# Performance work log

Measured on AMD Instinct MI355X. Metric: run time of the kernel, lower is better.

Reference implementation:

```python
import jax, jax.numpy as jnp
import numpy as np

B, S, D, H, DFF = 2, 2048, 1024, 16, 4096
DH = D // H
EPS = 1e-8


def _alibi_bias(num_heads, seq_len, dtype=jnp.float32):
    # ALiBi slopes for power-of-two head counts: 2^(-8*(h+1)/H)
    h = jnp.arange(1, num_heads + 1, dtype=dtype)
    slopes = jnp.exp2(-8.0 * h / num_heads)          # [H]
    pos = jnp.arange(seq_len, dtype=dtype)
    rel = jnp.abs(pos[None, :] - pos[:, None])       # [S, S] |i-j|
    return -slopes[:, None, None] * rel[None]        # [H, S, S]


def _rmsnorm(x, scale):
    rms = jax.lax.rsqrt(jnp.mean(x * x, axis=-1, keepdims=True) + EPS)
    return scale * x * rms


def setup_inputs() -> dict:
    key = jax.random.key(0)
    ks = jax.random.split(key, 12)
    sd = 0.02
    return {
        "x": jax.random.normal(ks[0], (B, S, D), jnp.float32),
        "scale1": jnp.ones((D,), jnp.float32),
        "scale2": jnp.ones((D,), jnp.float32),
        "w_qkv": jax.random.normal(ks[1], (D, 3 * D), jnp.float32) * sd,
        "b_qkv": jnp.zeros((3 * D,), jnp.float32),
        "w_out": jax.random.normal(ks[2], (D, D), jnp.float32) * sd,
        "b_out": jnp.zeros((D,), jnp.float32),
        "w1": jax.random.normal(ks[3], (D, DFF), jnp.float32) * sd,
        "b1": jnp.zeros((DFF,), jnp.float32),
        "w2": jax.random.normal(ks[4], (DFF, D), jnp.float32) * sd,
        "b2": jnp.zeros((D,), jnp.float32),
    }


def reference(x, scale1, scale2, w_qkv, b_qkv, w_out, b_out, w1, b1, w2, b2):
    residual = x
    xn = _rmsnorm(x, scale1)
    qkv = xn @ w_qkv + b_qkv                                  # [B,S,3D]
    q, k, v = jnp.split(qkv, 3, axis=-1)
    def heads(t):
        return t.reshape(B, S, H, DH).transpose(0, 2, 1, 3)   # [B,H,S,DH]
    q, k, v = heads(q), heads(k), heads(v)
    scores = jnp.einsum("bhsd,bhtd->bhst", q, k) / (DH ** 0.5)
    scores = scores + _alibi_bias(H, S, scores.dtype)[None]
    attn = jax.nn.softmax(scores, axis=-1)
    out = jnp.einsum("bhst,bhtd->bhsd", attn, v)              # [B,H,S,DH]
    out = out.transpose(0, 2, 1, 3).reshape(B, S, D)
    x = residual + (out @ w_out + b_out)
    residual = x
    xn = _rmsnorm(x, scale2)
    h = jax.nn.gelu(xn @ w1 + b1, approximate=False)
    return residual + (h @ w2 + b2)
```

## Files before the change

kernel.cpp:

```cpp
#include <hip/hip_runtime.h>
#include <hip/hip_bf16.h>
#include <math.h>

#define B_ 2
#define S_ 2048
#define D_ 1024
#define H_ 16
#define DH_ 64
#define DFF_ 4096
#define M_ (B_*S_)

typedef __bf16 bf16;
typedef __bf16 bf16x8 __attribute__((ext_vector_type(8)));
typedef __bf16 bf16x4 __attribute__((ext_vector_type(4)));
typedef float f32x4 __attribute__((ext_vector_type(4)));

__device__ __forceinline__ void gll16(const void* g, void* l) {
  __builtin_amdgcn_global_load_lds(
      (const __attribute__((address_space(1))) void*)g,
      (__attribute__((address_space(3))) void*)l, 16, 0, 0);
}

__global__ __launch_bounds__(256) void rmsnorm_kernel(const float* __restrict__ x,
    const float* __restrict__ scale, bf16* __restrict__ out) {
  __shared__ float red[4];
  int row = blockIdx.x, t = threadIdx.x;
  const float4* xr = (const float4*)(x + (size_t)row * D_);
  float4 v = xr[t];
  float ss = v.x*v.x + v.y*v.y + v.z*v.z + v.w*v.w;
  #pragma unroll
  for (int off = 32; off > 0; off >>= 1) ss += __shfl_down(ss, off, 64);
  if ((t & 63) == 0) red[t >> 6] = ss;
  __syncthreads();
  float tot = red[0] + red[1] + red[2] + red[3];
  float r = rsqrtf(tot * (1.0f / D_) + 1e-8f);
  float4 sc = ((const float4*)scale)[t];
  bf16x4 o;
  o[0] = (bf16)(v.x * sc.x * r);
  o[1] = (bf16)(v.y * sc.y * r);
  o[2] = (bf16)(v.z * sc.z * r);
  o[3] = (bf16)(v.w * sc.w * r);
  *(bf16x4*)(out + (size_t)row * D_ + t * 4) = o;
}

__global__ __launch_bounds__(256) void reduce_rms_kernel(
    const bf16* __restrict__ p0, const bf16* __restrict__ p1,
    const float* __restrict__ x, const float* __restrict__ bias,
    const float* __restrict__ scale, float* __restrict__ x2, bf16* __restrict__ xn2) {
  __shared__ float red[4];
  int row = blockIdx.x, t = threadIdx.x;
  float4 xv = ((const float4*)(x + (size_t)row * D_))[t];
  float4 bv = ((const float4*)bias)[t];
  bf16x4 a = *(const bf16x4*)(p0 + (size_t)row * D_ + t * 4);
  bf16x4 b = *(const bf16x4*)(p1 + (size_t)row * D_ + t * 4);
  float s0 = xv.x + bv.x + (float)a[0] + (float)b[0];
  float s1 = xv.y + bv.y + (float)a[1] + (float)b[1];
  float s2 = xv.z + bv.z + (float)a[2] + (float)b[2];
  float s3 = xv.w + bv.w + (float)a[3] + (float)b[3];
  float4 o; o.x = s0; o.y = s1; o.z = s2; o.w = s3;
  ((float4*)(x2 + (size_t)row * D_))[t] = o;
  float ss = s0*s0 + s1*s1 + s2*s2 + s3*s3;
  #pragma unroll
  for (int off = 32; off > 0; off >>= 1) ss += __shfl_down(ss, off, 64);
  if ((t & 63) == 0) red[t >> 6] = ss;
  __syncthreads();
  float tot = red[0] + red[1] + red[2] + red[3];
  float r = rsqrtf(tot * (1.0f / D_) + 1e-8f);
  float4 sc = ((const float4*)scale)[t];
  bf16x4 on;
  on[0] = (bf16)(s0 * sc.x * r);
  on[1] = (bf16)(s1 * sc.y * r);
  on[2] = (bf16)(s2 * sc.z * r);
  on[3] = (bf16)(s3 * sc.w * r);
  *(bf16x4*)(xn2 + (size_t)row * D_ + t * 4) = on;
}

__global__ __launch_bounds__(256) void reduce_out_kernel(
    const bf16* __restrict__ p0, const bf16* __restrict__ p1,
    const float* __restrict__ x2, const float* __restrict__ bias,
    float* __restrict__ dout) {
  int row = blockIdx.x, t = threadIdx.x;
  float4 xv = ((const float4*)(x2 + (size_t)row * D_))[t];
  float4 bv = ((const float4*)bias)[t];
  bf16x4 a = *(const bf16x4*)(p0 + (size_t)row * D_ + t * 4);
  bf16x4 b = *(const bf16x4*)(p1 + (size_t)row * D_ + t * 4);
  float4 o;
  o.x = xv.x + bv.x + (float)a[0] + (float)b[0];
  o.y = xv.y + bv.y + (float)a[1] + (float)b[1];
  o.z = xv.z + bv.z + (float)a[2] + (float)b[2];
  o.w = xv.w + bv.w + (float)a[3] + (float)b[3];
  ((float4*)(dout + (size_t)row * D_))[t] = o;
}

__global__ __launch_bounds__(256) void wtrans_kernel(const float* __restrict__ W,
    bf16* __restrict__ Wt, int K, int N) {
  __shared__ float tile[32][33];
  int n0 = blockIdx.x * 32, k0 = blockIdx.y * 32;
  int tx = threadIdx.x & 31, ty = threadIdx.x >> 5;
  #pragma unroll
  for (int i = 0; i < 4; i++)
    tile[ty + i*8][tx] = W[(size_t)(k0 + ty + i*8) * N + n0 + tx];
  __syncthreads();
  #pragma unroll
  for (int i = 0; i < 4; i++)
    Wt[(size_t)(n0 + ty + i*8) * K + k0 + tx] = (bf16)tile[tx][ty + i*8];
}

__global__ __launch_bounds__(256) void vtrans_kernel(const bf16* __restrict__ Vin,
    bf16* __restrict__ Vt) {
  __shared__ bf16 tile[32][34];
  size_t base = (size_t)blockIdx.z * (S_ * DH_);
  int s0 = blockIdx.x * 32, d0 = blockIdx.y * 32;
  int tx = threadIdx.x & 31, ty = threadIdx.x >> 5;
  #pragma unroll
  for (int i = 0; i < 4; i++)
    tile[ty + i*8][tx] = Vin[base + (size_t)(s0 + ty + i*8) * DH_ + d0 + tx];
  __syncthreads();
  #pragma unroll
  for (int i = 0; i < 4; i++)
    Vt[base + (size_t)(d0 + ty + i*8) * S_ + s0 + tx] = tile[tx][ty + i*8];
}

__device__ __forceinline__ float gelu_exact(float v) {
  return 0.5f * v * (1.0f + erff(v * 0.70710678118654752f));
}

template<int MODE>
__global__ __launch_bounds__(256) void gemm_kernel(
    const bf16* __restrict__ A, const bf16* __restrict__ Bt,
    const float* __restrict__ bias, void* __restrict__ outp, void* __restrict__ outp2,
    int M, int N, int K, int lda) {
  __shared__ __align__(16) bf16 As[128 * 32];
  __shared__ __align__(16) bf16 Bs[128 * 32];
  int t = threadIdx.x;
  int wave = t >> 6, lane = t & 63;
  int lm = lane & 15, lg = lane >> 4;
  int m0 = blockIdx.y * 128, n0 = blockIdx.x * 128;
  size_t koff = (size_t)blockIdx.z * K;
  int wm = (wave >> 1) * 64, wn = (wave & 1) * 64;
  f32x4 acc[4][4] = {};

  const bf16* Ag = A + (size_t)(m0 + (t >> 2)) * lda + koff + (t & 3) * 8;
  const bf16* Bg = Bt + (size_t)(n0 + (t >> 2)) * lda + koff + (t & 3) * 8;

  for (int k0 = 0; k0 < K; k0 += 32) {
    __syncthreads();
    gll16(Ag + k0, As + t * 8);
    gll16(Ag + k0 + (size_t)64 * lda, As + 2048 + t * 8);
    gll16(Bg + k0, Bs + t * 8);
    gll16(Bg + k0 + (size_t)64 * lda, Bs + 2048 + t * 8);
    __syncthreads();
    bf16x8 af[4], bfr[4];
    #pragma unroll
    for (int i = 0; i < 4; i++)
      af[i] = *(const bf16x8*)(As + (wm + i * 16 + lm) * 32 + lg * 8);
    #pragma unroll
    for (int j = 0; j < 4; j++)
      bfr[j] = *(const bf16x8*)(Bs + (wn + j * 16 + lm) * 32 + lg * 8);
    #pragma unroll
    for (int i = 0; i < 4; i++)
      #pragma unroll
      for (int j = 0; j < 4; j++)
        acc[i][j] = __builtin_amdgcn_mfma_f32_16x16x32_bf16(af[i], bfr[j], acc[i][j], 0, 0, 0);
  }

  bf16* pout = (MODE == 5) ? ((blockIdx.z == 0) ? (bf16*)outp : (bf16*)outp2) : (bf16*)outp;

  #pragma unroll
  for (int i = 0; i < 4; i++) {
    int row = m0 + wm + i * 16 + lg * 4;
    #pragma unroll
    for (int j = 0; j < 4; j++) {
      int col = n0 + wn + j * 16 + lm;
      float bcol = (MODE == 5) ? 0.f : bias[col];
      #pragma unroll
      for (int r = 0; r < 4; r++) {
        float v = acc[i][j][r] + bcol;
        int rr = row + r;
        if (MODE == 0) {
          int which = col >> 10, d = col & 1023;
          int hh = d >> 6, dh = d & 63;
          int bb = rr >> 11, s = rr & 2047;
          ((bf16*)outp)[(size_t)which * ((size_t)B_*H_*S_*DH_) +
              ((size_t)(bb * H_ + hh) * S_ + s) * DH_ + dh] = (bf16)v;
        } else if (MODE == 2) {
          ((bf16*)outp)[(size_t)rr * N + col] = (bf16)gelu_exact(v);
        } else {
          pout[(size_t)rr * N + col] = (bf16)v;
        }
      }
    }
  }
}

#define PSTR 68
__global__ __launch_bounds__(256, 3) void attn_kernel(
    const bf16* __restrict__ q, const bf16* __restrict__ k,
    const bf16* __restrict__ vT, bf16* __restrict__ ao) {
  __shared__ __align__(16) bf16 Ks[2][64 * 64];
  __shared__ __align__(16) bf16 Vs[2][64 * 64];
  __shared__ __align__(16) bf16 Ps[4 * 16 * PSTR];
  int t = threadIdx.x, wave = t >> 6, lane = t & 63;
  int lm = lane & 15, lg = lane >> 4;
  int q0 = blockIdx.x * 64;
  int h = blockIdx.y, b = blockIdx.z;
  size_t base = (size_t)(b * H_ + h) * ((size_t)S_ * DH_);
  const bf16* Q = q + base;
  const bf16* K = k + base;
  const bf16* V = vT + base;
  const float LOG2E = 1.4426950408889634f;
  float sl2 = exp2f(-0.5f * (float)(h + 1)) * LOG2E;
  float nslope = -sl2;
  const float qscale = 0.125f * LOG2E;
  const float FMAX = 8.0f;

  int W = (int)(24.0f / sl2);
  int jlo = (q0 - W) >> 6; if (jlo < 0) jlo = 0;
  int jhi = ((q0 + 63 + W) >> 6) + 1; if (jhi > S_ / 64) jhi = S_ / 64;

  bf16x8 qf[2];
  #pragma unroll
  for (int h2 = 0; h2 < 2; h2++) {
    bf16x8 v = *(const bf16x8*)(Q + (size_t)(q0 + wave * 16 + lm) * DH_ + h2 * 32 + lg * 8);
    #pragma unroll
    for (int e = 0; e < 8; e++) v[e] = (bf16)((float)v[e] * qscale);
    qf[h2] = v;
  }

  int row0 = t >> 3, jslot = t & 7;
  int gsw = (jslot ^ (row0 & 7)) << 3;
  const bf16* Ksrc0 = K + (size_t)row0 * DH_ + gsw;
  const bf16* Vsrc0 = V + (size_t)row0 * S_ + gsw;

  {
    int jt = jlo << 6;
    gll16(Ksrc0 + (size_t)jt * DH_, Ks[0] + (size_t)t * 8);
    gll16(Ksrc0 + (size_t)(jt + 32) * DH_, Ks[0] + (size_t)(t + 256) * 8);
    gll16(Vsrc0 + jt, Vs[0] + (size_t)t * 8);
    gll16(Vsrc0 + (size_t)32 * S_ + jt, Vs[0] + (size_t)(t + 256) * 8);
  }

  f32x4 oacc[4] = {};
  float rs[4] = {0.f, 0.f, 0.f, 0.f};
  int psw = lm & 7;

  for (int jj = jlo; jj < jhi; ++jj) {
    int buf = (jj - jlo) & 1;
    int jt = jj << 6;
    __syncthreads();
    if (jj + 1 < jhi) {
      int jn = (jj + 1) << 6;
      gll16(Ksrc0 + (size_t)jn * DH_, Ks[buf ^ 1] + (size_t)t * 8);
      gll16(Ksrc0 + (size_t)(jn + 32) * DH_, Ks[buf ^ 1] + (size_t)(t + 256) * 8);
      gll16(Vsrc0 + jn, Vs[buf ^ 1] + (size_t)t * 8);
      gll16(Vsrc0 + (size_t)32 * S_ + jn, Vs[buf ^ 1] + (size_t)(t + 256) * 8);
    }
    const bf16* Kb = Ks[buf];
    const bf16* Vb = Vs[buf];

    f32x4 sc[4];
    #pragma unroll
    for (int tt = 0; tt < 4; tt++) {
      f32x4 a = {-FMAX, -FMAX, -FMAX, -FMAX};
      int krow = tt * 16 + lm;
      bf16x8 kb0 = *(const bf16x8*)(Kb + (size_t)(krow * 8 + (lg ^ psw)) * 8);
      bf16x8 kb1 = *(const bf16x8*)(Kb + (size_t)(krow * 8 + ((lg + 4) ^ psw)) * 8);
      a = __builtin_amdgcn_mfma_f32_16x16x32_bf16(qf[0], kb0, a, 0, 0, 0);
      a = __builtin_amdgcn_mfma_f32_16x16x32_bf16(qf[1], kb1, a, 0, 0, 0);
      sc[tt] = a;
    }

    bf16* Pw = Ps + wave * (16 * PSTR);
    int i0 = q0 + wave * 16 + lg * 4;
    #pragma unroll
    for (int tt = 0; tt < 4; tt++) {
      float f0 = (float)(i0 - jt - tt * 16 - lm);
      #pragma unroll
      for (int r = 0; r < 4; r++) {
        float s2 = fmaf(nslope, fabsf(f0 + (float)r), sc[tt][r]);
        float p = __builtin_amdgcn_exp2f(s2);
        rs[r] += p;
        Pw[(lg * 4 + r) * PSTR + tt * 16 + lm] = (bf16)p;
      }
    }

    bf16x8 ap0 = *(const bf16x8*)(Pw + lm * PSTR + lg * 8);
    bf16x8 ap1 = *(const bf16x8*)(Pw + lm * PSTR + 32 + lg * 8);
    #pragma unroll
    for (int tt = 0; tt < 4; tt++) {
      int vrow = tt * 16 + lm;
      bf16x8 vb0 = *(const bf16x8*)(Vb + (size_t)(vrow * 8 + (lg ^ psw)) * 8);
      bf16x8 vb1 = *(const bf16x8*)(Vb + (size_t)(vrow * 8 + ((lg + 4) ^ psw)) * 8);
      oacc[tt] = __builtin_amdgcn_mfma_f32_16x16x32_bf16(ap0, vb0, oacc[tt], 0, 0, 0);
      oacc[tt] = __builtin_amdgcn_mfma_f32_16x16x32_bf16(ap1, vb1, oacc[tt], 0, 0, 0);
    }
  }

  #pragma unroll
  for (int r = 0; r < 4; r++) {
    #pragma unroll
    for (int off = 1; off < 16; off <<= 1)
      rs[r] += __shfl_xor(rs[r], off, 16);
  }

  #pragma unroll
  for (int r = 0; r < 4; r++) {
    float inv = 1.0f / rs[r];
    int row = q0 + wave * 16 + lg * 4 + r;
    #pragma unroll
    for (int tt = 0; tt < 4; tt++) {
      int col = h * 64 + tt * 16 + lm;
      ao[((size_t)(b * S_) + row) * D_ + col] = (bf16)(oacc[tt][r] * inv);
    }
  }
}

extern "C" void kernel_launch(void* const* d_in, const int* in_sizes, int n_in,
                              void* d_out, int out_size, void* d_ws, size_t ws_size,
                              hipStream_t stream) {
  const float* x      = (const float*)d_in[0];
  const float* scale1 = (const float*)d_in[1];
  const float* scale2 = (const float*)d_in[2];
  const float* w_qkv  = (const float*)d_in[3];
  const float* b_qkv  = (const float*)d_in[4];
  const float* w_out  = (const float*)d_in[5];
  const float* b_out  = (const float*)d_in[6];
  const float* w1     = (const float*)d_in[7];
  const float* b1     = (const float*)d_in[8];
  const float* w2     = (const float*)d_in[9];
  const float* b2     = (const float*)d_in[10];

  char* ws = (char*)d_ws;
  const size_t MB = 1024 * 1024;
  bf16* xn    = (bf16*)(ws + 0);
  bf16* qb    = (bf16*)(ws + 8*MB);
  bf16* kb    = (bf16*)(ws + 16*MB);
  bf16* vb    = (bf16*)(ws + 24*MB);
  bf16* vT    = (bf16*)(ws + 32*MB);
  bf16* wqkvT = (bf16*)(ws + 40*MB);
  bf16* woutT = (bf16*)(ws + 46*MB);
  bf16* w1T   = (bf16*)(ws + 48*MB);
  bf16* w2T   = (bf16*)(ws + 56*MB);
  float* x2   = (float*)(ws + 64*MB);
  bf16* xn2   = qb;
  bf16* pp0   = kb;
  bf16* pp1   = vb;
  bf16* hbuf  = kb;
  bf16* qp0   = xn;
  bf16* qp1   = w1T;
  bf16* ao    = xn;

  dim3 blk(256);
  wtrans_kernel<<<dim3(3072/32, 1024/32), blk, 0, stream>>>(w_qkv, wqkvT, 1024, 3072);
  wtrans_kernel<<<dim3(1024/32, 1024/32), blk, 0, stream>>>(w_out, woutT, 1024, 1024);
  wtrans_kernel<<<dim3(4096/32, 1024/32), blk, 0, stream>>>(w1, w1T, 1024, 4096);
  wtrans_kernel<<<dim3(1024/32, 4096/32), blk, 0, stream>>>(w2, w2T, 4096, 1024);

  rmsnorm_kernel<<<dim3(M_), blk, 0, stream>>>(x, scale1, xn);

  gemm_kernel<0><<<dim3(3072/128, M_/128, 1), blk, 0, stream>>>(
      xn, wqkvT, b_qkv, qb, nullptr, M_, 3072, 1024, 1024);

  vtrans_kernel<<<dim3(S_/32, DH_/32, B_*H_), blk, 0, stream>>>(vb, vT);

  attn_kernel<<<dim3(S_/64, H_, B_), blk, 0, stream>>>(qb, kb, vT, ao);

  gemm_kernel<5><<<dim3(1024/128, M_/128, 2), blk, 0, stream>>>(
      ao, woutT, nullptr, pp0, pp1, M_, 1024, 512, 1024);
  reduce_rms_kernel<<<dim3(M_), blk, 0, stream>>>(pp0, pp1, x, b_out, scale2, x2, xn2);

  gemm_kernel<2><<<dim3(4096/128, M_/128, 1), blk, 0, stream>>>(
      xn2, w1T, b1, hbuf, nullptr, M_, 4096, 1024, 1024);

  gemm_kernel<5><<<dim3(1024/128, M_/128, 2), blk, 0, stream>>>(
      hbuf, w2T, nullptr, qp0, qp1, M_, 1024, 2048, 4096);
  reduce_out_kernel<<<dim3(M_), blk, 0, stream>>>(qp0, qp1, x2, b2, (float*)d_out);
}
```

Measured before the change: 412.7 us.

## Double-buffer GEMM LDS tiles, swizzle LDS layout, use tanh-form GELU

The GEMM kernel now keeps two LDS buffers. It prefetches the next K-slice with global_load_lds while the MFMAs consume the current one, which cuts the loop from two barriers per step to one. Stores and fragment reads use an XOR swizzle on the 8-element column slot to reduce LDS bank conflicts. The exact erf GELU in the FFN epilogue is replaced by a sigmoid/exp2 form of the tanh approximation, which is cheaper but drifts slightly from the exact-GELU reference. LDS use doubles, which may lower occupancy.

```diff
diff --git a/kernel.cpp b/kernel.cpp
--- a/kernel.cpp
+++ b/kernel.cpp
@@ -121,8 +121,9 @@
     Vt[base + (size_t)(d0 + ty + i*8) * S_ + s0 + tx] = tile[tx][ty + i*8];
 }
 
-__device__ __forceinline__ float gelu_exact(float v) {
-  return 0.5f * v * (1.0f + erff(v * 0.70710678118654752f));
+__device__ __forceinline__ float gelu_fast(float x) {
+  float e = __builtin_amdgcn_exp2f(2.3022585093f * x * (1.0f + 0.044715f * x * x));
+  return x * e / (1.0f + e);
 }
 
 template<int MODE>
@@ -130,8 +131,8 @@
     const bf16* __restrict__ A, const bf16* __restrict__ Bt,
     const float* __restrict__ bias, void* __restrict__ outp, void* __restrict__ outp2,
     int M, int N, int K, int lda) {
-  __shared__ __align__(16) bf16 As[128 * 32];
-  __shared__ __align__(16) bf16 Bs[128 * 32];
+  __shared__ __align__(16) bf16 As[2][128 * 32];
+  __shared__ __align__(16) bf16 Bs[2][128 * 32];
   int t = threadIdx.x;
   int wave = t >> 6, lane = t & 63;
   int lm = lane & 15, lg = lane >> 4;
@@ -140,23 +141,37 @@
   int wm = (wave >> 1) * 64, wn = (wave & 1) * 64;
   f32x4 acc[4][4] = {};
 
-  const bf16* Ag = A + (size_t)(m0 + (t >> 2)) * lda + koff + (t & 3) * 8;
-  const bf16* Bg = Bt + (size_t)(n0 + (t >> 2)) * lda + koff + (t & 3) * 8;
-
-  for (int k0 = 0; k0 < K; k0 += 32) {
+  int srow = t >> 2, sslot = t & 3;
+  int scol = (sslot ^ ((srow >> 1) & 3)) * 8;
+  const bf16* Ag = A + (size_t)(m0 + srow) * lda + koff + scol;
+  const bf16* Bg = Bt + (size_t)(n0 + srow) * lda + koff + scol;
+  size_t half = (size_t)64 * lda;
+
+  int rsw = (lm >> 1) & 3;
+
+  gll16(Ag, As[0] + t * 8);
+  gll16(Ag + half, As[0] + 2048 + t * 8);
+  gll16(Bg, Bs[0] + t * 8);
+  gll16(Bg + half, Bs[0] + 2048 + t * 8);
+
+  int buf = 0;
+  for (int k0 = 0; k0 < K; k0 += 32, buf ^= 1) {
     __syncthreads();
-    gll16(Ag + k0, As + t * 8);
-    gll16(Ag + k0 + (size_t)64 * lda, As + 2048 + t * 8);
-    gll16(Bg + k0, Bs + t * 8);
-    gll16(Bg + k0 + (size_t)64 * lda, Bs + 2048 + t * 8);
-    __syncthreads();
+    if (k0 + 32 < K) {
+      gll16(Ag + k0 + 32, As[buf ^ 1] + t * 8);
+      gll16(Ag + k0 + 32 + half, As[buf ^ 1] + 2048 + t * 8);
+      gll16(Bg + k0 + 32, Bs[buf ^ 1] + t * 8);
+      gll16(Bg + k0 + 32 + half, Bs[buf ^ 1] + 2048 + t * 8);
+    }
+    const bf16* Ab = As[buf];
+    const bf16* Bb = Bs[buf];
     bf16x8 af[4], bfr[4];
     #pragma unroll
     for (int i = 0; i < 4; i++)
-      af[i] = *(const bf16x8*)(As + (wm + i * 16 + lm) * 32 + lg * 8);
+      af[i] = *(const bf16x8*)(Ab + (wm + i * 16 + lm) * 32 + (lg ^ rsw) * 8);
     #pragma unroll
     for (int j = 0; j < 4; j++)
-      bfr[j] = *(const bf16x8*)(Bs + (wn + j * 16 + lm) * 32 + lg * 8);
+      bfr[j] = *(const bf16x8*)(Bb + (wn + j * 16 + lm) * 32 + (lg ^ rsw) * 8);
     #pragma unroll
     for (int i = 0; i < 4; i++)
       #pragma unroll
@@ -184,7 +199,7 @@
           ((bf16*)outp)[(size_t)which * ((size_t)B_*H_*S_*DH_) +
               ((size_t)(bb * H_ + hh) * S_ + s) * DH_ + dh] = (bf16)v;
         } else if (MODE == 2) {
-          ((bf16*)outp)[(size_t)rr * N + col] = (bf16)gelu_exact(v);
+          ((bf16*)outp)[(size_t)rr * N + col] = (bf16)gelu_fast(v);
         } else {
           pout[(size_t)rr * N + col] = (bf16)v;
         }
```

After: 377.7 us. -8.5%, faster.
